# Optimization experiments

Measured on AMD Instinct MI355X. Metric: run time of the kernel, lower is better.

Reference implementation:

```python
import jax, jax.numpy as jnp
import numpy as np

EPS = 1e-7
B, C, IMG = 1024, 3, 32
NCLASS = 10
N_IN, L_IN, L_OUT = 64, 16, 16   # primary caps: 64 capsules of length 16; digit caps length 16
R_ITER = 3


def squash(c, axis):
    dot = jnp.sum(c * c, axis=axis, keepdims=True)
    return dot / (1.0 + dot) / jnp.sqrt(dot + EPS) * c


def conv2d(x, w, b, stride):
    y = jax.lax.conv_general_dilated(x, w, (stride, stride), 'VALID',
                                     dimension_numbers=('NCHW', 'OIHW', 'NCHW'))
    return y + b[None, :, None, None]


def setup_inputs() -> dict:
    key = jax.random.key(0)
    ks = jax.random.split(key, 16)
    inp = {
        'x': jax.random.uniform(ks[0], (B, C, IMG, IMG), dtype=jnp.float32),
        'y': jax.random.randint(ks[1], (B,), 0, NCLASS, dtype=jnp.int64),
        'conv1_w': 0.05 * jax.random.normal(ks[2], (128, C, 3, 3), jnp.float32),
        'conv1_b': jnp.zeros((128,), jnp.float32),
        'conv2_w': 0.05 * jax.random.normal(ks[3], (256, 128, 5, 5), jnp.float32),
        'conv2_b': jnp.zeros((256,), jnp.float32),
        'conv3_w': 0.05 * jax.random.normal(ks[4], (256, 256, 5, 5), jnp.float32),
        'conv3_b': jnp.zeros((256,), jnp.float32),
        'caps_w': 0.05 * jax.random.normal(ks[5], (N_IN, NCLASS, L_IN, L_OUT), jnp.float32),
        'caps_b': 0.05 * jax.random.normal(ks[6], (NCLASS, L_OUT), jnp.float32),
        'fc1_w': 0.05 * jax.random.normal(ks[7], (512, NCLASS * L_OUT), jnp.float32),
        'fc1_b': jnp.zeros((512,), jnp.float32),
        'fc2_w': 0.05 * jax.random.normal(ks[8], (1024, 512), jnp.float32),
        'fc2_b': jnp.zeros((1024,), jnp.float32),
        'fc3_w': 0.05 * jax.random.normal(ks[9], (IMG * IMG * C, 1024), jnp.float32),
        'fc3_b': jnp.zeros((IMG * IMG * C,), jnp.float32),
    }
    return inp


def reference(x, y, conv1_w, conv1_b, conv2_w, conv2_b, conv3_w, conv3_b,
              caps_w, caps_b, fc1_w, fc1_b, fc2_w, fc2_b, fc3_w, fc3_b):
    # CNN blocks
    h = jax.nn.relu(conv2d(x, conv1_w, conv1_b, 2))   # [B,128,15,15]
    h = jax.nn.relu(conv2d(h, conv2_w, conv2_b, 2))   # [B,256,6,6]
    h = jax.nn.relu(conv2d(h, conv3_w, conv3_b, 1))   # [B,256,2,2]

    # Primary capsules: [B,64,16], squashed along capsule-length axis
    prim = squash(h.reshape(h.shape[0], N_IN, L_IN), axis=-1)

    # u_hat[b,i,o,j] = sum_k W[i,o,k,j] * prim[b,i,k]  -> [B,64,10,16]
    u_hat = jnp.einsum('bik,iokj->bioj', prim, caps_w)
    u_hat_det = jax.lax.stop_gradient(u_hat)

    b_ij = jnp.zeros((h.shape[0], N_IN, NCLASS), dtype=u_hat.dtype)
    v = None
    for r in range(R_ITER):
        c_ij = jax.nn.softmax(b_ij, axis=2)           # over output capsules
        uh = u_hat if r == R_ITER - 1 else u_hat_det
        s = jnp.einsum('bio,bioj->boj', c_ij, uh) + caps_b   # [B,10,16]
        v = squash(s, axis=-1)
        if r < R_ITER - 1:
            agree = jnp.einsum('bioj,boj->bio', u_hat_det, jax.lax.stop_gradient(v))
            b_ij = b_ij + agree

    # capsule lengths: [B,10,1,1]
    v_lengths = jnp.sqrt(jnp.sum(v * v, axis=-1, keepdims=True) + EPS)[..., None]

    # reconstruction (mask by true label one-hot)
    one_hot = jax.nn.one_hot(y, NCLASS, dtype=v.dtype)       # [B,10]
    masked = (v * one_hot[:, :, None]).reshape(v.shape[0], NCLASS * L_OUT)
    h1 = jax.nn.relu(masked @ fc1_w.T + fc1_b)
    h2 = jax.nn.relu(h1 @ fc2_w.T + fc2_b)
    decoded = jax.nn.sigmoid(h2 @ fc3_w.T + fc3_b)           # [B,3072]
    return (v_lengths, decoded)
```

## Files before the change

### kernel.cpp

```cpp
#include <hip/hip_runtime.h>
#include <hip/hip_bf16.h>
#include <math.h>

#define EPSF 1e-7f

typedef __attribute__((ext_vector_type(8))) short bhalf8;
typedef __attribute__((ext_vector_type(4))) float floatx4;

__global__ __launch_bounds__(256) void conv1_kernel(
    const float* __restrict__ x, const float* __restrict__ w,
    const float* __restrict__ bias, __hip_bfloat16* __restrict__ out)
{
  const int b0 = blockIdx.x * 2;
  const int t = threadIdx.x;
  if (t >= 225) return;
  const int py = t / 15, px = t % 15;
  float win[2][27];
#pragma unroll
  for (int im = 0; im < 2; ++im) {
    const float* xb = x + (size_t)(b0 + im) * 3072;
#pragma unroll
    for (int c = 0; c < 3; ++c)
#pragma unroll
      for (int ky = 0; ky < 3; ++ky)
#pragma unroll
        for (int kx = 0; kx < 3; ++kx)
          win[im][c*9 + ky*3 + kx] = xb[c*1024 + (py*2 + ky)*32 + (px*2 + kx)];
  }
#pragma unroll 1
  for (int oc0 = 0; oc0 < 128; oc0 += 32) {
    __hip_bfloat16 hv[2][32];
#pragma unroll
    for (int oc = 0; oc < 32; ++oc) {
      const float* wp = &w[(oc0 + oc)*27];
      float a0 = bias[oc0 + oc], a1 = a0;
#pragma unroll
      for (int q = 0; q < 27; ++q) {
        a0 = fmaf(win[0][q], wp[q], a0);
        a1 = fmaf(win[1][q], wp[q], a1);
      }
      hv[0][oc] = __float2bfloat16(fmaxf(a0, 0.f));
      hv[1][oc] = __float2bfloat16(fmaxf(a1, 0.f));
    }
#pragma unroll
    for (int qq = 0; qq < 4; ++qq) {
      int c16 = (oc0 >> 3) + qq;
#pragma unroll
      for (int im = 0; im < 2; ++im) {
        const uint4* src = (const uint4*)hv[im];
        *(uint4*)((char*)out + (size_t)(b0+im)*57600 + c16*3600 + t*16) = src[qq];
      }
    }
  }
}

__global__ __launch_bounds__(256) void prep_kernel(
    const float* __restrict__ conv2w, const float* __restrict__ conv3w,
    const float* __restrict__ capsw,  const float* __restrict__ fc1w,
    const float* __restrict__ fc2w,   const float* __restrict__ fc3w,
    __hip_bfloat16* __restrict__ wt2, __hip_bfloat16* __restrict__ wt3,
    __hip_bfloat16* __restrict__ cwt, float* __restrict__ fc1wt,
    __hip_bfloat16* __restrict__ wf2, __hip_bfloat16* __restrict__ wf3)
{
  __shared__ float tl[6400];
  const int t = threadIdx.x;
  int b = blockIdx.x;
  if (b < 12288) {
    int i = b*256 + t;
    wf3[i] = __float2bfloat16(fc3w[i]);
    return;
  }
  b -= 12288;
  if (b < 2048) {
    int i = b*256 + t;
    wf2[i] = __float2bfloat16(fc2w[i]);
    return;
  }
  b -= 2048;
  if (b < 640) {
    int i2 = b*256 + t;
    int k = i2 & 15, j = (i2 >> 4) & 15, io = i2 >> 8;
    cwt[i2] = __float2bfloat16(capsw[(io*16 + k)*16 + j]);
    return;
  }
  b -= 640;
  if (b < 320) {
    int i = b*256 + t;
    int j = i >> 9, n = i & 511;
    fc1wt[i] = fc1w[n*160 + j];
    return;
  }
  b -= 320;
  if (b < 256) {
    const float* src = conv3w + (size_t)b*6400;
    for (int i = t; i < 6400; i += 256) tl[i] = src[i];
    __syncthreads();
#pragma unroll 1
    for (int q = 0; q < 25; ++q) {
      int j = q*256 + t;
      int s = j >> 6, kq = j & 63;
      int tap = j >> 8, ic = j & 255;
      wt3[(size_t)s*16384 + b*64 + kq] = __float2bfloat16(tl[ic*25 + tap]);
    }
    return;
  }
  b -= 256;
  {
    const float* src = conv2w + (size_t)b*3200;
    for (int i = t; i < 3200; i += 256) tl[i] = src[i];
    __syncthreads();
#pragma unroll 1
    for (int q = 0; q < 13; ++q) {
      int j = q*256 + t;
      if (j < 3200) {
        int s = j >> 5, kq = j & 31;
        int h = (s >= 50) ? 1 : 0;
        int r2 = s - h*50;
        int tap = r2 >> 1, qq = r2 & 1;
        int ic = h*64 + qq*32 + kq;
        wt2[(size_t)s*8192 + b*32 + kq] = __float2bfloat16(tl[ic*25 + tap]);
      }
    }
  }
}

__global__ __launch_bounds__(512) void conv2_mfma_v5_kernel(
    const __hip_bfloat16* __restrict__ a,
    const __hip_bfloat16* __restrict__ wt,
    const float* __restrict__ bias,
    __hip_bfloat16* __restrict__ out,
    int img_base)
{
  __shared__ __align__(16) unsigned short Il[2*225*64];
  const int b0   = img_base + blockIdx.x * 2;
  const int t    = threadIdx.x;
  const int lane = t & 63;
  const int w    = t >> 6;
  const int wm   = w >> 2;
  const int wn   = w & 3;
  const int n    = lane & 15;
  const int g    = lane >> 4;

  const char* gB = (const char*)wt + (wn*64 + n)*64 + g*16;
  bhalf8 bs0[4], bs1[4];
#pragma unroll
  for (int nt = 0; nt < 4; ++nt) {
    bs0[nt] = *(const bhalf8*)(gB + nt*1024);
    bs1[nt] = *(const bhalf8*)(gB + 16384 + nt*1024);
  }

  const int tbase = wm*3;
  int Abase[3], em[3];
#pragma unroll
  for (int mt = 0; mt < 3; ++mt) {
    int tile = tbase + mt;
    int m = tile*16 + n;
    if (m >= 72) m = 0;
    int img = m / 36, pos = m - img*36;
    int py = pos / 6, px = pos - py*6;
    int pixb = 30*py + 2*px;
    Abase[mt] = (img*225 + pixb) * 128;
    em[mt] = g + m;
  }

  floatx4 acc[3][4];
#pragma unroll
  for (int mt = 0; mt < 3; ++mt)
#pragma unroll
    for (int nt = 0; nt < 4; ++nt)
      acc[mt][nt] = (floatx4){0.f, 0.f, 0.f, 0.f};

  int s = 0;
#pragma unroll 1
  for (int h = 0; h < 2; ++h) {
    if (h) __syncthreads();
    for (int i = t; i < 3600; i += 512) {
      int img = i / 1800;
      int r = i - img*1800;
      int p = r >> 3, c = r & 7;
      uint4 v = *(const uint4*)((const char*)a +
                (size_t)(b0+img)*57600 + (h*8 + c)*3600 + p*16);
      int px15 = p % 15, py15 = p / 15;
      int csw = (c + (px15 >> 1) + 6*(py15 >> 1) + (img << 2)) & 7;
      *(uint4*)((char*)Il + (img*225 + p)*128 + csw*16) = v;
    }
    __syncthreads();

    int dpix = 0, kx = 0, ky = 0;
#pragma unroll 1
    for (int tap = 0; tap < 25; ++tap) {
      const int doff = dpix << 7;
      const int dsw  = (kx >> 1) + 6*(ky >> 1);
      int a0[3];
#pragma unroll
      for (int mt = 0; mt < 3; ++mt)
        a0[mt] = Abase[mt] + doff + (((em[mt] + dsw) & 7) << 4);

#pragma unroll
      for (int mt = 0; mt < 2; ++mt) {
        bhalf8 av = *(const bhalf8*)((const char*)Il + a0[mt]);
#pragma unroll
        for (int nt = 0; nt < 4; ++nt)
          acc[mt][nt] = __builtin_amdgcn_mfma_f32_16x16x32_bf16(av, bs0[nt], acc[mt][nt], 0, 0, 0);
      }
      if (wm == 0) {
        bhalf8 av = *(const bhalf8*)((const char*)Il + a0[2]);
#pragma unroll
        for (int nt = 0; nt < 4; ++nt)
          acc[2][nt] = __builtin_amdgcn_mfma_f32_16x16x32_bf16(av, bs0[nt], acc[2][nt], 0, 0, 0);
      }
      {
        const int spre = (s + 2 < 100) ? (s + 2) : 99;
#pragma unroll
        for (int nt = 0; nt < 4; ++nt)
          bs0[nt] = *(const bhalf8*)(gB + (size_t)spre*16384 + nt*1024);
      }
#pragma unroll
      for (int mt = 0; mt < 2; ++mt) {
        bhalf8 av = *(const bhalf8*)((const char*)Il + (a0[mt] ^ 64));
#pragma unroll
        for (int nt = 0; nt < 4; ++nt)
          acc[mt][nt] = __builtin_amdgcn_mfma_f32_16x16x32_bf16(av, bs1[nt], acc[mt][nt], 0, 0, 0);
      }
      if (wm == 0) {
        bhalf8 av = *(const bhalf8*)((const char*)Il + (a0[2] ^ 64));
#pragma unroll
        for (int nt = 0; nt < 4; ++nt)
          acc[2][nt] = __builtin_amdgcn_mfma_f32_16x16x32_bf16(av, bs1[nt], acc[2][nt], 0, 0, 0);
      }
      {
        const int spre = (s + 3 < 100) ? (s + 3) : 99;
#pragma unroll
        for (int nt = 0; nt < 4; ++nt)
          bs1[nt] = *(const bhalf8*)(gB + (size_t)spre*16384 + nt*1024);
      }
      s += 2;
      if (kx == 4) { kx = 0; ++ky; dpix += 11; } else { ++kx; ++dpix; }
    }
  }

  float bv[4];
#pragma unroll
  for (int nt = 0; nt < 4; ++nt) bv[nt] = bias[wn*64 + nt*16 + n];
#pragma unroll
  for (int mt = 0; mt < 3; ++mt) {
    if (mt < 2 || wm == 0) {
      int tile = tbase + mt;
#pragma unroll
      for (int r = 0; r < 4; ++r) {
        int m = tile*16 + g*4 + r;
        if (m < 72) {
          int img = m / 36, pos = m - img*36;
          size_t o = (((size_t)(b0+img)*36 + pos) << 8) + wn*64 + n;
#pragma unroll
          for (int nt = 0; nt < 4; ++nt)
            out[o + nt*16] = __float2bfloat16(fmaxf(acc[mt][nt][r] + bv[nt], 0.f));
        }
      }
    }
  }
}

__global__ __launch_bounds__(512) void conv3_mfma_kernel(
    const __hip_bfloat16* __restrict__ a,
    const __hip_bfloat16* __restrict__ wt,
    float* __restrict__ pout)
{
  __shared__ __align__(16) unsigned short Il[16*1448];
  const int b0   = blockIdx.x * 16;
  const int kq   = blockIdx.y;
  const int t    = threadIdx.x;
  const int lane = t & 63;
  const int w    = t >> 6;
  const int n    = lane & 15;
  const int g    = lane >> 4;

  for (int i = t; i < 2304; i += 512) {
    int img = i / 144, r = i - img*144;
    int p = r >> 2, c = r & 3;
    uint4 v = *(const uint4*)((const char*)a +
              ((((size_t)(b0+img)*36 + p) << 9) + kq*64 + c*16));
    *(uint4*)((char*)Il + (img*1448 + p*40 + c*8)*2) = v;
  }

  const char* gB = (const char*)wt + (size_t)(w*32 + n)*128 +
                   (kq & 1)*64 + g*16;
  const int kqs = kq >> 1;
  bhalf8 b00, b01, b10, b11;
  b00 = *(const bhalf8*)(gB + (size_t)(0*4 + kqs)*32768);
  b01 = *(const bhalf8*)(gB + (size_t)(0*4 + kqs)*32768 + 2048);
  b10 = *(const bhalf8*)(gB + (size_t)(1*4 + kqs)*32768);
  b11 = *(const bhalf8*)(gB + (size_t)(1*4 + kqs)*32768 + 2048);

  const int d = n >> 2, pos = n & 3;
  const int pb = (pos >> 1)*6 + (pos & 1);
  int ab[4];
#pragma unroll
  for (int mt = 0; mt < 4; ++mt)
    ab[mt] = ((mt*4 + d)*1448 + pb*40 + g*8) * 2;

  floatx4 acc[4][2];
#pragma unroll
  for (int mt = 0; mt < 4; ++mt)
#pragma unroll
    for (int nt = 0; nt < 2; ++nt)
      acc[mt][nt] = (floatx4){0.f, 0.f, 0.f, 0.f};

  __syncthreads();

  int toff = 0, kx = 0;
#pragma unroll 1
  for (int tap = 0; tap < 24; tap += 2) {
#pragma unroll
    for (int mt = 0; mt < 4; ++mt) {
      bhalf8 av = *(const bhalf8*)((const char*)Il + ab[mt] + toff*80);
      acc[mt][0] = __builtin_amdgcn_mfma_f32_16x16x32_bf16(av, b00, acc[mt][0], 0, 0, 0);
      acc[mt][1] = __builtin_amdgcn_mfma_f32_16x16x32_bf16(av, b01, acc[mt][1], 0, 0, 0);
    }
    b00 = *(const bhalf8*)(gB + (size_t)((tap+2)*4 + kqs)*32768);
    b01 = *(const bhalf8*)(gB + (size_t)((tap+2)*4 + kqs)*32768 + 2048);
    if (++kx == 5) { kx = 0; toff += 2; } else ++toff;
#pragma unroll
    for (int mt = 0; mt < 4; ++mt) {
      bhalf8 av = *(const bhalf8*)((const char*)Il + ab[mt] + toff*80);
      acc[mt][0] = __builtin_amdgcn_mfma_f32_16x16x32_bf16(av, b10, acc[mt][0], 0, 0, 0);
      acc[mt][1] = __builtin_amdgcn_mfma_f32_16x16x32_bf16(av, b11, acc[mt][1], 0, 0, 0);
    }
    {
      const int tpre = (tap + 3 <= 24) ? (tap + 3) : 24;
      b10 = *(const bhalf8*)(gB + (size_t)(tpre*4 + kqs)*32768);
      b11 = *(const bhalf8*)(gB + (size_t)(tpre*4 + kqs)*32768 + 2048);
    }
    if (++kx == 5) { kx = 0; toff += 2; } else ++toff;
  }
#pragma unroll
  for (int mt = 0; mt < 4; ++mt) {
    bhalf8 av = *(const bhalf8*)((const char*)Il + ab[mt] + toff*80);
    acc[mt][0] = __builtin_amdgcn_mfma_f32_16x16x32_bf16(av, b00, acc[mt][0], 0, 0, 0);
    acc[mt][1] = __builtin_amdgcn_mfma_f32_16x16x32_bf16(av, b01, acc[mt][1], 0, 0, 0);
  }

  float* po = pout + (size_t)kq*1048576;
#pragma unroll
  for (int mt = 0; mt < 4; ++mt) {
#pragma unroll
    for (int r = 0; r < 4; ++r) {
      int m = mt*16 + g*4 + r;
      int img = m >> 2, p2 = m & 3;
#pragma unroll
      for (int nt = 0; nt < 2; ++nt)
        po[((size_t)(b0+img)*256 + w*32 + nt*16 + n)*4 + p2] = acc[mt][nt][r];
    }
  }
}

__global__ __launch_bounds__(256) void caps_kernel(
    const float* __restrict__ pout, const __hip_bfloat16* __restrict__ cwt,
    const float* __restrict__ cb, const float* __restrict__ c3b,
    const int* __restrict__ y,
    const float* __restrict__ fc1wt, const float* __restrict__ fc1b,
    float* __restrict__ vlen, __hip_bfloat16* __restrict__ h1f)
{
  __shared__ float prim[1024];
  __shared__ float uh[10240];
  __shared__ float bij[640];
  __shared__ float cij[640];
  __shared__ float vv[160];
  const int b = blockIdx.x, t = threadIdx.x;
  {
    const float* pp = pout + (size_t)b*1024 + t*4;
    float4 s4 = *(const float4*)pp;
#pragma unroll
    for (int q = 1; q < 8; ++q) {
      float4 v = *(const float4*)(pp + (size_t)q*1048576);
      s4.x += v.x; s4.y += v.y; s4.z += v.z; s4.w += v.w;
    }
    const float bv = c3b[t];
    float4 h = make_float4(fmaxf(s4.x + bv, 0.f), fmaxf(s4.y + bv, 0.f),
                           fmaxf(s4.z + bv, 0.f), fmaxf(s4.w + bv, 0.f));
    float dd = h.x*h.x + h.y*h.y + h.z*h.z + h.w*h.w;
    dd += __shfl_xor(dd, 1);
    dd += __shfl_xor(dd, 2);
    float sc = dd / (1.f + dd) / sqrtf(dd + EPSF);
    float4 o4 = make_float4(h.x*sc, h.y*sc, h.z*sc, h.w*sc);
    *(float4*)&prim[t*4] = o4;
  }
  for (int f = t; f < 640; f += 256) bij[f] = 0.f;
  __syncthreads();
  for (int f = t; f < 10240; f += 256) {
    const int i = f / 160;
    const uint4* wv = (const uint4*)(cwt + (size_t)f*16);
    uint4 wa = wv[0], wb = wv[1];
    unsigned uw[8] = {wa.x, wa.y, wa.z, wa.w, wb.x, wb.y, wb.z, wb.w};
    const float* pp = prim + i*16;
    float s = 0.f;
#pragma unroll
    for (int q = 0; q < 8; ++q) {
      float lo = __uint_as_float(uw[q] << 16);
      float hi = __uint_as_float(uw[q] & 0xffff0000u);
      s = fmaf(pp[2*q],   lo, s);
      s = fmaf(pp[2*q+1], hi, s);
    }
    uh[f] = s;
  }
  __syncthreads();
  for (int r = 0; r < 3; ++r) {
    if (t < 64) {
      float e[10];
      float mx = -1e30f;
#pragma unroll
      for (int o = 0; o < 10; ++o) { e[o] = bij[t*10 + o]; mx = fmaxf(mx, e[o]); }
      float sum = 0.f;
#pragma unroll
      for (int o = 0; o < 10; ++o) { e[o] = expf(e[o] - mx); sum += e[o]; }
      float inv = 1.f / sum;
#pragma unroll
      for (int o = 0; o < 10; ++o) cij[t*10 + o] = e[o] * inv;
    }
    __syncthreads();
    if (t < 160) {
      const int o = t >> 4;
      float s0 = cb[t], s1 = 0.f, s2 = 0.f, s3 = 0.f;
      for (int i = 0; i < 64; i += 4) {
        s0 = fmaf(cij[(i+0)*10 + o], uh[(i+0)*160 + t], s0);
        s1 = fmaf(cij[(i+1)*10 + o], uh[(i+1)*160 + t], s1);
        s2 = fmaf(cij[(i+2)*10 + o], uh[(i+2)*160 + t], s2);
        s3 = fmaf(cij[(i+3)*10 + o], uh[(i+3)*160 + t], s3);
      }
      float s = (s0 + s1) + (s2 + s3);
      float dd = s*s;
      dd += __shfl_xor(dd, 1); dd += __shfl_xor(dd, 2);
      dd += __shfl_xor(dd, 4); dd += __shfl_xor(dd, 8);
      float sc = dd / (1.f + dd) / sqrtf(dd + EPSF);
      vv[t] = s * sc;
      if (r == 2 && (t & 15) == 0)
        vlen[b*10 + o] = sqrtf(sc*sc*dd + EPSF);
    }
    __syncthreads();
    if (r < 2) {
      for (int f = t; f < 640; f += 256) {
        int i = f / 10, o = f % 10;
        const float* up = &uh[i*160 + o*16];
        const float* vp = &vv[o*16];
        float a = 0.f;
#pragma unroll
        for (int j = 0; j < 16; ++j) a = fmaf(up[j], vp[j], a);
        bij[f] += a;
      }
      __syncthreads();
    }
  }
  const int yb = y[b];
  const float* vy = &vv[yb*16];
  for (int nn = t; nn < 512; nn += 256) {
    float s = fc1b[nn];
#pragma unroll
    for (int k = 0; k < 16; ++k)
      s = fmaf(vy[k], fc1wt[(yb*16 + k)*512 + nn], s);
    h1f[b*512 + nn] = __float2bfloat16(fmaxf(s, 0.f));
  }
}

template<int ACT, int MT, int NT>
__global__ __launch_bounds__(256) void fc_mfma_kernel(
    const __hip_bfloat16* __restrict__ A,
    const __hip_bfloat16* __restrict__ W,
    const float* __restrict__ bias,
    void* __restrict__ outv, int M, int N, int K)
{
  const int t    = threadIdx.x;
  const int lane = t & 63;
  const int w    = t >> 6;
  const int wr   = w >> 1, wc = w & 1;
  const int n    = lane & 15, g = lane >> 4;
  const int m0   = blockIdx.x * (2*MT*16) + wr*(MT*16);
  const int n0   = blockIdx.y * (2*NT*16) + wc*(NT*16);
  const __hip_bfloat16* Ap = A + (size_t)(m0 + n)*K + g*8;
  const __hip_bfloat16* Wp = W + (size_t)(n0 + n)*K + g*8;
  const int steps = K >> 5;

  bhalf8 aa0[MT], aa1[MT], bb0[NT], bb1[NT];
#pragma unroll
  for (int mt = 0; mt < MT; ++mt) {
    aa0[mt] = *(const bhalf8*)(Ap + (size_t)mt*16*K);
    aa1[mt] = *(const bhalf8*)(Ap + (size_t)mt*16*K + 32);
  }
#pragma unroll
  for (int nt = 0; nt < NT; ++nt) {
    bb0[nt] = *(const bhalf8*)(Wp + (size_t)nt*16*K);
    bb1[nt] = *(const bhalf8*)(Wp + (size_t)nt*16*K + 32);
  }

  floatx4 acc[MT][NT];
#pragma unroll
  for (int mt = 0; mt < MT; ++mt)
#pragma unroll
    for (int nt = 0; nt < NT; ++nt)
      acc[mt][nt] = (floatx4){0.f, 0.f, 0.f, 0.f};

#pragma unroll 1
  for (int s = 0; s < steps; s += 2) {
#pragma unroll
    for (int mt = 0; mt < MT; ++mt)
#pragma unroll
      for (int nt = 0; nt < NT; ++nt)
        acc[mt][nt] = __builtin_amdgcn_mfma_f32_16x16x32_bf16(
            aa0[mt], bb0[nt], acc[mt][nt], 0, 0, 0);
    {
      const int spre = (s + 2 < steps) ? (s + 2) : s;
#pragma unroll
      for (int mt = 0; mt < MT; ++mt)
        aa0[mt] = *(const bhalf8*)(Ap + (size_t)mt*16*K + spre*32);
#pragma unroll
      for (int nt = 0; nt < NT; ++nt)
        bb0[nt] = *(const bhalf8*)(Wp + (size_t)nt*16*K + spre*32);
    }
#pragma unroll
    for (int mt = 0; mt < MT; ++mt)
#pragma unroll
      for (int nt = 0; nt < NT; ++nt)
        acc[mt][nt] = __builtin_amdgcn_mfma_f32_16x16x32_bf16(
            aa1[mt], bb1[nt], acc[mt][nt], 0, 0, 0);
    {
      const int spre = (s + 3 < steps) ? (s + 3) : (s + 1);
#pragma unroll
      for (int mt = 0; mt < MT; ++mt)
        aa1[mt] = *(const bhalf8*)(Ap + (size_t)mt*16*K + spre*32);
#pragma unroll
      for (int nt = 0; nt < NT; ++nt)
        bb1[nt] = *(const bhalf8*)(Wp + (size_t)nt*16*K + spre*32);
    }
  }

#pragma unroll
  for (int mt = 0; mt < MT; ++mt) {
#pragma unroll
    for (int r = 0; r < 4; ++r) {
      const int m = m0 + mt*16 + g*4 + r;
#pragma unroll
      for (int nt = 0; nt < NT; ++nt) {
        const int col = n0 + nt*16 + n;
        float v = acc[mt][nt][r] + bias[col];
        if (ACT == 0) {
          ((__hip_bfloat16*)outv)[(size_t)m*N + col] =
              __float2bfloat16(fmaxf(v, 0.f));
        } else {
          ((float*)outv)[(size_t)m*N + col] = 1.f / (1.f + expf(-v));
        }
      }
    }
  }
}

extern "C" void kernel_launch(void* const* d_in, const int* in_sizes, int n_in,
                              void* d_out, int out_size, void* d_ws, size_t ws_size,
                              hipStream_t stream) {
  const float* x       = (const float*)d_in[0];
  const int*   y       = (const int*)  d_in[1];
  const float* conv1_w = (const float*)d_in[2];
  const float* conv1_b = (const float*)d_in[3];
  const float* conv2_w = (const float*)d_in[4];
  const float* conv2_b = (const float*)d_in[5];
  const float* conv3_w = (const float*)d_in[6];
  const float* conv3_b = (const float*)d_in[7];
  const float* caps_w  = (const float*)d_in[8];
  const float* caps_b  = (const float*)d_in[9];
  const float* fc1_w   = (const float*)d_in[10];
  const float* fc1_b   = (const float*)d_in[11];
  const float* fc2_w   = (const float*)d_in[12];
  const float* fc2_b   = (const float*)d_in[13];
  const float* fc3_w   = (const float*)d_in[14];
  const float* fc3_b   = (const float*)d_in[15];
  float* out = (float*)d_out;
  float* ws  = (float*)d_ws;

  __hip_bfloat16* h1t   = (__hip_bfloat16*)ws;
  __hip_bfloat16* wt2   = (__hip_bfloat16*)(ws + 14745600);
  __hip_bfloat16* wt3   = (__hip_bfloat16*)(ws + 15155200);
  __hip_bfloat16* h2t   = (__hip_bfloat16*)(ws + 15974400);
  float*          pout  = ws + 20692992;
  __hip_bfloat16* h1f   = (__hip_bfloat16*)(ws + 29081600);
  __hip_bfloat16* h2f   = (__hip_bfloat16*)(ws + 29343744);
  __hip_bfloat16* wf2   = (__hip_bfloat16*)(ws + 29868032);
  __hip_bfloat16* wf3   = (__hip_bfloat16*)(ws + 30130176);
  __hip_bfloat16* cwt   = (__hip_bfloat16*)(ws + 31703040);
  float*          fc1wt = ws + 31784960;

  prep_kernel<<<dim3(15808), 256, 0, stream>>>(
      conv2_w, conv3_w, caps_w, fc1_w, fc2_w, fc3_w,
      wt2, wt3, cwt, fc1wt, wf2, wf3);
  conv1_kernel<<<dim3(512),        256, 0, stream>>>(x, conv1_w, conv1_b, h1t);
  conv2_mfma_v5_kernel<<<dim3(512), 512, 0, stream>>>(h1t, wt2, conv2_b, h2t, 0);
  conv3_mfma_kernel<<<dim3(64, 8), 512, 0, stream>>>(h2t, wt3, pout);
  caps_kernel<<<dim3(1024),        256, 0, stream>>>(pout, cwt, caps_b, conv3_b,
                                                     y, fc1wt, fc1_b, out, h1f);
  fc_mfma_kernel<0,2,2><<<dim3(16, 16), 256, 0, stream>>>(
      h1f, wf2, fc2_b, h2f, 1024, 1024, 512);
  fc_mfma_kernel<1,2,2><<<dim3(16, 48), 256, 0, stream>>>(
      h2f, wf3, fc3_b, out + 10240, 1024, 3072, 1024);
}
```

Measured before the change: 402.5 us.

## Fuse conv1 into prep kernel and widen conv2 blocks to four images

Conv1 now runs inside the weight-prep kernel as its first 512 blocks, which removes one launch. It also stages the conv1 weights and bias in shared memory with padded float4 reads. Conv2 now processes four images per block with 768 threads (12 waves, 144 rows exactly in 9 M-tiles), which removes the partial-tile branching and halves the block count while sharing B-fragment loads across more rows. Each conv2 block needs more LDS and more registers, so occupancy may fall, and conv1 now shares a kernel with the bandwidth-bound conversion work.

```diff
diff --git a/kernel.cpp b/kernel.cpp
--- a/kernel.cpp
+++ b/kernel.cpp
@@ -7,54 +7,9 @@
 typedef __attribute__((ext_vector_type(8))) short bhalf8;
 typedef __attribute__((ext_vector_type(4))) float floatx4;
 
-__global__ __launch_bounds__(256) void conv1_kernel(
-    const float* __restrict__ x, const float* __restrict__ w,
-    const float* __restrict__ bias, __hip_bfloat16* __restrict__ out)
-{
-  const int b0 = blockIdx.x * 2;
-  const int t = threadIdx.x;
-  if (t >= 225) return;
-  const int py = t / 15, px = t % 15;
-  float win[2][27];
-#pragma unroll
-  for (int im = 0; im < 2; ++im) {
-    const float* xb = x + (size_t)(b0 + im) * 3072;
-#pragma unroll
-    for (int c = 0; c < 3; ++c)
-#pragma unroll
-      for (int ky = 0; ky < 3; ++ky)
-#pragma unroll
-        for (int kx = 0; kx < 3; ++kx)
-          win[im][c*9 + ky*3 + kx] = xb[c*1024 + (py*2 + ky)*32 + (px*2 + kx)];
-  }
-#pragma unroll 1
-  for (int oc0 = 0; oc0 < 128; oc0 += 32) {
-    __hip_bfloat16 hv[2][32];
-#pragma unroll
-    for (int oc = 0; oc < 32; ++oc) {
-      const float* wp = &w[(oc0 + oc)*27];
-      float a0 = bias[oc0 + oc], a1 = a0;
-#pragma unroll
-      for (int q = 0; q < 27; ++q) {
-        a0 = fmaf(win[0][q], wp[q], a0);
-        a1 = fmaf(win[1][q], wp[q], a1);
-      }
-      hv[0][oc] = __float2bfloat16(fmaxf(a0, 0.f));
-      hv[1][oc] = __float2bfloat16(fmaxf(a1, 0.f));
-    }
-#pragma unroll
-    for (int qq = 0; qq < 4; ++qq) {
-      int c16 = (oc0 >> 3) + qq;
-#pragma unroll
-      for (int im = 0; im < 2; ++im) {
-        const uint4* src = (const uint4*)hv[im];
-        *(uint4*)((char*)out + (size_t)(b0+im)*57600 + c16*3600 + t*16) = src[qq];
-      }
-    }
-  }
-}
-
-__global__ __launch_bounds__(256) void prep_kernel(
+__global__ __launch_bounds__(256) void prepc1_kernel(
+    const float* __restrict__ x,      const float* __restrict__ conv1w,
+    const float* __restrict__ conv1b, __hip_bfloat16* __restrict__ h1t,
     const float* __restrict__ conv2w, const float* __restrict__ conv3w,
     const float* __restrict__ capsw,  const float* __restrict__ fc1w,
     const float* __restrict__ fc2w,   const float* __restrict__ fc3w,
@@ -62,9 +17,66 @@
     __hip_bfloat16* __restrict__ cwt, float* __restrict__ fc1wt,
     __hip_bfloat16* __restrict__ wf2, __hip_bfloat16* __restrict__ wf3)
 {
-  __shared__ float tl[6400];
+  __shared__ float sh[6400];
   const int t = threadIdx.x;
   int b = blockIdx.x;
+
+  if (b < 512) {
+    float* wl = sh;
+    float* bl = sh + 4096;
+    const int b0 = b * 2;
+    for (int i = t; i < 4096; i += 256) {
+      int oc = i >> 5, q = i & 31;
+      wl[i] = (q < 27) ? conv1w[oc*27 + q] : 0.f;
+    }
+    if (t < 128) bl[t] = conv1b[t];
+    __syncthreads();
+    if (t >= 225) return;
+    const int py = t / 15, px = t % 15;
+    float win[2][28];
+    win[0][27] = 0.f; win[1][27] = 0.f;
+#pragma unroll
+    for (int im = 0; im < 2; ++im) {
+      const float* xb = x + (size_t)(b0 + im) * 3072;
+#pragma unroll
+      for (int c = 0; c < 3; ++c)
+#pragma unroll
+        for (int ky = 0; ky < 3; ++ky)
+#pragma unroll
+          for (int kx = 0; kx < 3; ++kx)
+            win[im][c*9 + ky*3 + kx] = xb[c*1024 + (py*2 + ky)*32 + (px*2 + kx)];
+    }
+#pragma unroll 1
+    for (int oc0 = 0; oc0 < 128; oc0 += 32) {
+      __hip_bfloat16 hv[2][32];
+#pragma unroll
+      for (int oc = 0; oc < 32; ++oc) {
+        const float4* wp = (const float4*)&wl[(oc0 + oc) << 5];
+        float a0 = bl[oc0 + oc], a1 = a0;
+#pragma unroll
+        for (int qq = 0; qq < 7; ++qq) {
+          float4 wv = wp[qq];
+          a0 = fmaf(win[0][qq*4+0], wv.x, a0); a1 = fmaf(win[1][qq*4+0], wv.x, a1);
+          a0 = fmaf(win[0][qq*4+1], wv.y, a0); a1 = fmaf(win[1][qq*4+1], wv.y, a1);
+          a0 = fmaf(win[0][qq*4+2], wv.z, a0); a1 = fmaf(win[1][qq*4+2], wv.z, a1);
+          a0 = fmaf(win[0][qq*4+3], wv.w, a0); a1 = fmaf(win[1][qq*4+3], wv.w, a1);
+        }
+        hv[0][oc] = __float2bfloat16(fmaxf(a0, 0.f));
+        hv[1][oc] = __float2bfloat16(fmaxf(a1, 0.f));
+      }
+#pragma unroll
+      for (int qq = 0; qq < 4; ++qq) {
+        int c16 = (oc0 >> 3) + qq;
+#pragma unroll
+        for (int im = 0; im < 2; ++im) {
+          const uint4* src = (const uint4*)hv[im];
+          *(uint4*)((char*)h1t + (size_t)(b0+im)*57600 + c16*3600 + t*16) = src[qq];
+        }
+      }
+    }
+    return;
+  }
+  b -= 512;
   if (b < 12288) {
     int i = b*256 + t;
     wf3[i] = __float2bfloat16(fc3w[i]);
@@ -92,6 +104,7 @@
   }
   b -= 320;
   if (b < 256) {
+    float* tl = sh;
     const float* src = conv3w + (size_t)b*6400;
     for (int i = t; i < 6400; i += 256) tl[i] = src[i];
     __syncthreads();
@@ -106,6 +119,7 @@
   }
   b -= 256;
   {
+    float* tl = sh;
     const float* src = conv2w + (size_t)b*3200;
     for (int i = t; i < 3200; i += 256) tl[i] = src[i];
     __syncthreads();
@@ -124,15 +138,14 @@
   }
 }
 
-__global__ __launch_bounds__(512) void conv2_mfma_v5_kernel(
+__global__ __launch_bounds__(768) void conv2_mfma_v6_kernel(
     const __hip_bfloat16* __restrict__ a,
     const __hip_bfloat16* __restrict__ wt,
     const float* __restrict__ bias,
-    __hip_bfloat16* __restrict__ out,
-    int img_base)
+    __hip_bfloat16* __restrict__ out)
 {
-  __shared__ __align__(16) unsigned short Il[2*225*64];
-  const int b0   = img_base + blockIdx.x * 2;
+  __shared__ __align__(16) unsigned short Il[4*225*64];
+  const int b0   = blockIdx.x * 4;
   const int t    = threadIdx.x;
   const int lane = t & 63;
   const int w    = t >> 6;
@@ -149,13 +162,11 @@
     bs1[nt] = *(const bhalf8*)(gB + 16384 + nt*1024);
   }
 
-  const int tbase = wm*3;
   int Abase[3], em[3];
 #pragma unroll
   for (int mt = 0; mt < 3; ++mt) {
-    int tile = tbase + mt;
+    int tile = wm*3 + mt;
     int m = tile*16 + n;
-    if (m >= 72) m = 0;
     int img = m / 36, pos = m - img*36;
     int py = pos / 6, px = pos - py*6;
     int pixb = 30*py + 2*px;
@@ -174,14 +185,14 @@
 #pragma unroll 1
   for (int h = 0; h < 2; ++h) {
     if (h) __syncthreads();
-    for (int i = t; i < 3600; i += 512) {
+    for (int i = t; i < 7200; i += 768) {
       int img = i / 1800;
       int r = i - img*1800;
       int p = r >> 3, c = r & 7;
       uint4 v = *(const uint4*)((const char*)a +
                 (size_t)(b0+img)*57600 + (h*8 + c)*3600 + p*16);
       int px15 = p % 15, py15 = p / 15;
-      int csw = (c + (px15 >> 1) + 6*(py15 >> 1) + (img << 2)) & 7;
+      int csw = (c + (px15 >> 1) + 6*(py15 >> 1) + ((img & 1) << 2)) & 7;
       *(uint4*)((char*)Il + (img*225 + p)*128 + csw*16) = v;
     }
     __syncthreads();
@@ -197,18 +208,12 @@
         a0[mt] = Abase[mt] + doff + (((em[mt] + dsw) & 7) << 4);
 
 #pragma unroll
-      for (int mt = 0; mt < 2; ++mt) {
+      for (int mt = 0; mt < 3; ++mt) {
         bhalf8 av = *(const bhalf8*)((const char*)Il + a0[mt]);
 #pragma unroll
         for (int nt = 0; nt < 4; ++nt)
           acc[mt][nt] = __builtin_amdgcn_mfma_f32_16x16x32_bf16(av, bs0[nt], acc[mt][nt], 0, 0, 0);
       }
-      if (wm == 0) {
-        bhalf8 av = *(const bhalf8*)((const char*)Il + a0[2]);
-#pragma unroll
-        for (int nt = 0; nt < 4; ++nt)
-          acc[2][nt] = __builtin_amdgcn_mfma_f32_16x16x32_bf16(av, bs0[nt], acc[2][nt], 0, 0, 0);
-      }
       {
         const int spre = (s + 2 < 100) ? (s + 2) : 99;
 #pragma unroll
@@ -216,18 +221,12 @@
           bs0[nt] = *(const bhalf8*)(gB + (size_t)spre*16384 + nt*1024);
       }
 #pragma unroll
-      for (int mt = 0; mt < 2; ++mt) {
+      for (int mt = 0; mt < 3; ++mt) {
         bhalf8 av = *(const bhalf8*)((const char*)Il + (a0[mt] ^ 64));
 #pragma unroll
         for (int nt = 0; nt < 4; ++nt)
           acc[mt][nt] = __builtin_amdgcn_mfma_f32_16x16x32_bf16(av, bs1[nt], acc[mt][nt], 0, 0, 0);
       }
-      if (wm == 0) {
-        bhalf8 av = *(const bhalf8*)((const char*)Il + (a0[2] ^ 64));
-#pragma unroll
-        for (int nt = 0; nt < 4; ++nt)
-          acc[2][nt] = __builtin_amdgcn_mfma_f32_16x16x32_bf16(av, bs1[nt], acc[2][nt], 0, 0, 0);
-      }
       {
         const int spre = (s + 3 < 100) ? (s + 3) : 99;
 #pragma unroll
@@ -244,19 +243,15 @@
   for (int nt = 0; nt < 4; ++nt) bv[nt] = bias[wn*64 + nt*16 + n];
 #pragma unroll
   for (int mt = 0; mt < 3; ++mt) {
-    if (mt < 2 || wm == 0) {
-      int tile = tbase + mt;
-#pragma unroll
-      for (int r = 0; r < 4; ++r) {
-        int m = tile*16 + g*4 + r;
-        if (m < 72) {
-          int img = m / 36, pos = m - img*36;
-          size_t o = (((size_t)(b0+img)*36 + pos) << 8) + wn*64 + n;
-#pragma unroll
-          for (int nt = 0; nt < 4; ++nt)
-            out[o + nt*16] = __float2bfloat16(fmaxf(acc[mt][nt][r] + bv[nt], 0.f));
-        }
-      }
+    int tile = wm*3 + mt;
+#pragma unroll
+    for (int r = 0; r < 4; ++r) {
+      int m = tile*16 + g*4 + r;
+      int img = m / 36, pos = m - img*36;
+      size_t o = (((size_t)(b0+img)*36 + pos) << 8) + wn*64 + n;
+#pragma unroll
+      for (int nt = 0; nt < 4; ++nt)
+        out[o + nt*16] = __float2bfloat16(fmaxf(acc[mt][nt][r] + bv[nt], 0.f));
     }
   }
 }
@@ -586,11 +581,11 @@
   __hip_bfloat16* cwt   = (__hip_bfloat16*)(ws + 31703040);
   float*          fc1wt = ws + 31784960;
 
-  prep_kernel<<<dim3(15808), 256, 0, stream>>>(
+  prepc1_kernel<<<dim3(16320), 256, 0, stream>>>(
+      x, conv1_w, conv1_b, h1t,
       conv2_w, conv3_w, caps_w, fc1_w, fc2_w, fc3_w,
       wt2, wt3, cwt, fc1wt, wf2, wf3);
-  conv1_kernel<<<dim3(512),        256, 0, stream>>>(x, conv1_w, conv1_b, h1t);
-  conv2_mfma_v5_kernel<<<dim3(512), 512, 0, stream>>>(h1t, wt2, conv2_b, h2t, 0);
+  conv2_mfma_v6_kernel<<<dim3(256), 768, 0, stream>>>(h1t, wt2, conv2_b, h2t);
   conv3_mfma_kernel<<<dim3(64, 8), 512, 0, stream>>>(h2t, wt3, pout);
   caps_kernel<<<dim3(1024),        256, 0, stream>>>(pout, cwt, caps_b, conv3_b,
                                                      y, fc1wt, fc1_b, out, h1f);
```

Measured after the change: 349.5 us. 13.2% less time.
